# Optimization experiments

Hardware: AMD Instinct MI355X
Metric: run time of the kernel (lower is better)

## Reference

```python
import jax, jax.numpy as jnp
import numpy as np

D = 768
SCALE = 1.0 / np.sqrt(D)  # 1/sqrt(question_size)
NEG_INF = -1e30


def setup_inputs() -> dict:
    key = jax.random.key(0)
    k1, k2, k3, k4 = jax.random.split(key, 4)
    B, Lc, Lq = 8, 2048, 1024
    context_hiddens = jax.random.normal(k1, (B, Lc, D), dtype=jnp.float32)
    context_mask = jnp.ones((B, Lc), dtype=jnp.float32)  # unused by forward (parity with original)
    question_hiddens = jax.random.normal(k2, (B, Lq, D), dtype=jnp.float32)
    question_mask = jax.random.randint(k3, (B, Lq), 0, 2, dtype=jnp.int32)
    # ensure at least one valid question token per row to avoid all -inf softmax
    question_mask = question_mask.at[:, 0].set(1)
    W = jax.random.normal(k4, (D, D), dtype=jnp.float32) * (1.0 / np.sqrt(D))
    b = jnp.zeros((D,), dtype=jnp.float32)
    return {
        "context_hiddens": context_hiddens,
        "context_mask": context_mask,
        "question_hiddens": question_hiddens,
        "question_mask": question_mask,
        "W": W,
        "b": b,
    }


def reference(context_hiddens, context_mask, question_hiddens, question_mask, W, b):
    # Linear projection of question hiddens: [B, Lq, D]
    query = jnp.einsum("bqd,ed->bqe", question_hiddens, W) + b
    # Bilinear scores: c_i' W q_j -> [B, Lc, Lq], scaled
    scores = jnp.einsum("bcd,bqd->bcq", context_hiddens, query) * SCALE
    # Masked softmax over question axis (mask==1 means valid)
    mask = question_mask[:, None, :].astype(jnp.bool_)  # [B, 1, Lq]
    scores = jnp.where(mask, scores, NEG_INF)
    attention_dist = jax.nn.softmax(scores, axis=2)
    # Weighted sum of question hiddens: [B, Lc, D]
    attn_output = jnp.einsum("bcq,bqd->bcd", attention_dist, question_hiddens)
    return jnp.concatenate([context_hiddens, attn_output], axis=2)  # [B, Lc, 2D]
```

## Files before the change

### kernel.cpp

```cpp
#include <hip/hip_runtime.h>
#include <hip/hip_bf16.h>
#include <cstdint>
#include <cstddef>

#define D 768
#define BATCH 8
#define LC 2048
#define LQ 1024
#define SCALE 0.03608439182435161f

typedef __attribute__((ext_vector_type(8))) short short8;
typedef __attribute__((ext_vector_type(4))) float floatx4;

__device__ __forceinline__ short f2bf(float f) {
    union { float f; uint32_t u; } v; v.f = f;
    uint32_t r = v.u + 0x7fffu + ((v.u >> 16) & 1u);
    return (short)(r >> 16);
}

__device__ __forceinline__ void gl_lds16(const short* g, short* l) {
    __builtin_amdgcn_global_load_lds(
        reinterpret_cast<const __attribute__((address_space(1))) unsigned int*>(
            reinterpret_cast<uintptr_t>(g)),
        reinterpret_cast<__attribute__((address_space(3))) unsigned int*>(
            reinterpret_cast<uintptr_t>(l)),
        16, 0, 0);
}

__device__ __forceinline__ void stage_tile(const short* gbase, int ld, int m0, int k0,
                                           short* lds, int tid) {
    const int r = tid >> 2, kc = (tid & 3) * 8;
    gl_lds16(gbase + (size_t)(m0 + r) * ld + k0 + kc, lds + tid * 8);
    gl_lds16(gbase + (size_t)(m0 + r + 64) * ld + k0 + kc, lds + 2048 + tid * 8);
}

__device__ __forceinline__ void mfma_tile_loop(
    const short* Ab, const short* Bb, int lda, int ldb, int K, int m0, int n0,
    short* sA, short* sB, int tid, floatx4 acc[4][4]) {
    const int w = tid >> 6, lane = tid & 63, l15 = lane & 15, quad = lane >> 4;
    const int wm = (w >> 1) * 64, wn = (w & 1) * 64;
    for (int k0 = 0; k0 < K; k0 += 32) {
        stage_tile(Ab, lda, m0, k0, sA, tid);
        stage_tile(Bb, ldb, n0, k0, sB, tid);
        __syncthreads();
        short8 af[4], bf[4];
#pragma unroll
        for (int mt = 0; mt < 4; ++mt)
            af[mt] = *reinterpret_cast<const short8*>(&sA[(wm + mt * 16 + l15) * 32 + quad * 8]);
#pragma unroll
        for (int nt = 0; nt < 4; ++nt)
            bf[nt] = *reinterpret_cast<const short8*>(&sB[(wn + nt * 16 + l15) * 32 + quad * 8]);
#pragma unroll
        for (int mt = 0; mt < 4; ++mt)
#pragma unroll
            for (int nt = 0; nt < 4; ++nt)
                acc[mt][nt] = __builtin_amdgcn_mfma_f32_16x16x32_bf16(af[mt], bf[nt], acc[mt][nt], 0, 0, 0);
        __syncthreads();
    }
}

__device__ __forceinline__ void gemm256_loop(
    const short* __restrict__ A, const short* __restrict__ B,
    int lda, int ldb, int K, int m0, int n0,
    short* lds, int tid, floatx4 acc[8][4]) {
    const int lane = tid & 63, l15 = lane & 15, quad = lane >> 4;
    const int w = tid >> 6, wm = w >> 2, wn = w & 3;

    const int c0 = tid, c1 = tid + 512;
    const int r0 = c0 >> 2, s0 = (c0 & 3) ^ (r0 & 3);
    const int r1 = c1 >> 2, s1 = (c1 & 3) ^ (r1 & 3);
    const short* gA0 = A + (size_t)(m0 + r0) * lda + s0 * 8;
    const short* gA1 = A + (size_t)(m0 + r1) * lda + s1 * 8;
    const short* gB0 = B + (size_t)(n0 + r0) * ldb + s0 * 8;
    const short* gB1 = B + (size_t)(n0 + r1) * ldb + s1 * 8;
    short* dA0 = lds + c0 * 8;
    short* dA1 = lds + c1 * 8;
    short* dB0 = lds + 8192 + c0 * 8;
    short* dB1 = lds + 8192 + c1 * 8;

    int aoff[8], boff[4];
#pragma unroll
    for (int mt = 0; mt < 8; ++mt) {
        int r = wm * 128 + mt * 16 + l15;
        aoff[mt] = r * 32 + ((quad ^ (r & 3)) * 8);
    }
#pragma unroll
    for (int nt = 0; nt < 4; ++nt) {
        int r = wn * 64 + nt * 16 + l15;
        boff[nt] = 8192 + r * 32 + ((quad ^ (r & 3)) * 8);
    }

    const int NT = K >> 5;
#define STAGE_A(t, bb) { gl_lds16(gA0 + (t) * 32, dA0 + (bb)); gl_lds16(gA1 + (t) * 32, dA1 + (bb)); }
#define STAGE_B(t, bb) { gl_lds16(gB0 + (t) * 32, dB0 + (bb)); gl_lds16(gB1 + (t) * 32, dB1 + (bb)); }
    STAGE_A(0, 0) STAGE_B(0, 0)
    STAGE_A(1, 16384) STAGE_B(1, 16384)

    for (int kt = 0; kt < NT; ++kt) {
        const int cur = (kt % 3) * 16384;
        const int nxt = ((kt + 2) % 3) * 16384;
        if (kt + 1 < NT) { asm volatile("s_waitcnt vmcnt(4)" ::: "memory"); }
        else             { asm volatile("s_waitcnt vmcnt(0)" ::: "memory"); }
        __builtin_amdgcn_s_barrier();
        __builtin_amdgcn_sched_barrier(0);

        if (kt + 2 < NT) STAGE_A((kt + 2), nxt)

        short8 af[8], bf[4];
#pragma unroll
        for (int mt = 0; mt < 8; ++mt)
            af[mt] = *reinterpret_cast<const short8*>(lds + cur + aoff[mt]);
#pragma unroll
        for (int nt = 0; nt < 2; ++nt)
            bf[nt] = *reinterpret_cast<const short8*>(lds + cur + boff[nt]);
        __builtin_amdgcn_s_setprio(1);
#pragma unroll
        for (int mt = 0; mt < 8; ++mt)
#pragma unroll
            for (int nt = 0; nt < 2; ++nt)
                acc[mt][nt] = __builtin_amdgcn_mfma_f32_16x16x32_bf16(af[mt], bf[nt], acc[mt][nt], 0, 0, 0);
        __builtin_amdgcn_s_setprio(0);

        if (kt + 2 < NT) STAGE_B((kt + 2), nxt)

#pragma unroll
        for (int nt = 2; nt < 4; ++nt)
            bf[nt] = *reinterpret_cast<const short8*>(lds + cur + boff[nt]);
        __builtin_amdgcn_s_setprio(1);
#pragma unroll
        for (int mt = 0; mt < 8; ++mt)
#pragma unroll
            for (int nt = 2; nt < 4; ++nt)
                acc[mt][nt] = __builtin_amdgcn_mfma_f32_16x16x32_bf16(af[mt], bf[nt], acc[mt][nt], 0, 0, 0);
        __builtin_amdgcn_s_setprio(0);
        __builtin_amdgcn_sched_barrier(0);
    }
#undef STAGE_A
#undef STAGE_B
}

__global__ void cast_w_kernel(const float* __restrict__ src, short* __restrict__ dst,
                              float* __restrict__ sums) {
    int i = blockIdx.x * 256 + threadIdx.x;
    if (i < 4096) {
        float4 z = {0.f, 0.f, 0.f, 0.f};
        reinterpret_cast<float4*>(sums)[i] = z;
    }
    float4 v = reinterpret_cast<const float4*>(src)[i];
    short4 o;
    o.x = f2bf(v.x); o.y = f2bf(v.y); o.z = f2bf(v.z); o.w = f2bf(v.w);
    reinterpret_cast<short4*>(dst)[i] = o;
}

__global__ void qh_pass_kernel(const float* __restrict__ qh, short* __restrict__ qh_b,
                               short* __restrict__ qhT) {
    __shared__ float tile[32][33];
    const int b = blockIdx.z;
    const int q0 = blockIdx.x * 32, d0 = blockIdx.y * 32;
    const int t = threadIdx.x;
    const int r = t >> 3, c = (t & 7) * 4;
    const float4 v = *reinterpret_cast<const float4*>(qh + ((size_t)b * LQ + q0 + r) * D + d0 + c);
    tile[r][c] = v.x; tile[r][c + 1] = v.y; tile[r][c + 2] = v.z; tile[r][c + 3] = v.w;
    short4 d;
    d.x = f2bf(v.x); d.y = f2bf(v.y); d.z = f2bf(v.z); d.w = f2bf(v.w);
    *reinterpret_cast<short4*>(qh_b + ((size_t)b * LQ + q0 + r) * D + d0 + c) = d;
    __syncthreads();
    short4 o;
    o.x = f2bf(tile[c][r]); o.y = f2bf(tile[c + 1][r]);
    o.z = f2bf(tile[c + 2][r]); o.w = f2bf(tile[c + 3][r]);
    *reinterpret_cast<short4*>(qhT + ((size_t)b * D + d0 + r) * LQ + q0 + c) = o;
}

__global__ __launch_bounds__(256, 2) void gemm1_kernel(
    const short* __restrict__ A, const short* __restrict__ W,
    const float* __restrict__ bias, short* __restrict__ Q) {
    __shared__ short sA[128 * 32];
    __shared__ short sB[128 * 32];
    const int m0 = blockIdx.x * 128, n0 = blockIdx.y * 128;
    const int tid = threadIdx.x;
    const int w = tid >> 6, lane = tid & 63, l15 = lane & 15, quad = lane >> 4;
    const int wm = (w >> 1) * 64, wn = (w & 1) * 64;
    floatx4 acc[4][4];
#pragma unroll
    for (int i = 0; i < 4; ++i)
#pragma unroll
        for (int j = 0; j < 4; ++j) { floatx4 z = {0.f, 0.f, 0.f, 0.f}; acc[i][j] = z; }
    mfma_tile_loop(A, W, D, D, D, m0, n0, sA, sB, tid, acc);
    float bv[4];
#pragma unroll
    for (int nt = 0; nt < 4; ++nt) bv[nt] = bias[n0 + wn + nt * 16 + l15];
#pragma unroll
    for (int mt = 0; mt < 4; ++mt)
#pragma unroll
        for (int r = 0; r < 4; ++r) {
            int row = m0 + wm + mt * 16 + quad * 4 + r;
#pragma unroll
            for (int nt = 0; nt < 4; ++nt)
                Q[(size_t)row * D + n0 + wn + nt * 16 + l15] = f2bf(acc[mt][nt][r] + bv[nt]);
        }
}

__global__ void ctx_pass_kernel(const float* __restrict__ ctx, float* __restrict__ out,
                                short* __restrict__ ctxb) {
    size_t i = (size_t)blockIdx.x * 256 + threadIdx.x;
    size_t row = i / 192;
    size_t c4 = i % 192;
    float4 v = reinterpret_cast<const float4*>(ctx)[i];
    reinterpret_cast<float4*>(out)[row * 384 + c4] = v;
    short4 o;
    o.x = f2bf(v.x); o.y = f2bf(v.y); o.z = f2bf(v.z); o.w = f2bf(v.w);
    reinterpret_cast<short4*>(ctxb)[i] = o;
}

__global__ __launch_bounds__(512, 2) void scores256_kernel(
    const short* __restrict__ ctxb, const short* __restrict__ query_b,
    const int* __restrict__ qmask, short* __restrict__ P, float* __restrict__ sums) {
    __shared__ __align__(16) short lds[3 * 16384];
    const int nb = ((blockIdx.x & 7) << 5) + (blockIdx.x >> 3);
    const int b = nb >> 5, rem = nb & 31, by = rem >> 3, bx = rem & 7;
    const int m0 = bx << 8, n0 = by << 8;
    const int tid = threadIdx.x;
    const int lane = tid & 63, l15 = lane & 15, quad = lane >> 4;
    const int w = tid >> 6, wm = w >> 2, wn = w & 3;

    floatx4 acc[8][4];
#pragma unroll
    for (int i = 0; i < 8; ++i)
#pragma unroll
        for (int j = 0; j < 4; ++j) { floatx4 z = {0.f, 0.f, 0.f, 0.f}; acc[i][j] = z; }

    gemm256_loop(ctxb + (size_t)b * LC * D, query_b + (size_t)b * LQ * D,
                 D, D, D, m0, n0, lds, tid, acc);

    const int* mk = qmask + b * LQ;
    bool valid[4];
#pragma unroll
    for (int nt = 0; nt < 4; ++nt) valid[nt] = (mk[n0 + wn * 64 + nt * 16 + l15] != 0);
    short* Pb = P + (size_t)b * LC * LQ;
    float* sumb = sums + (size_t)b * LC;
#pragma unroll
    for (int mt = 0; mt < 8; ++mt)
#pragma unroll
        for (int rr = 0; rr < 4; ++rr) {
            int row = m0 + wm * 128 + mt * 16 + quad * 4 + rr;
            float psum = 0.f;
#pragma unroll
            for (int nt = 0; nt < 4; ++nt) {
                float pv = valid[nt] ? __expf(acc[mt][nt][rr] * SCALE) : 0.f;
                psum += pv;
                Pb[(size_t)row * LQ + n0 + wn * 64 + nt * 16 + l15] = f2bf(pv);
            }
#pragma unroll
            for (int off = 1; off < 16; off <<= 1)
                psum += __shfl_xor(psum, off, 64);
            if (l15 == 0)
                atomicAdd(&sumb[row], psum);
        }
}

__global__ __launch_bounds__(512, 2) void gemm2_256_kernel(
    const short* __restrict__ P, const short* __restrict__ qhT,
    const float* __restrict__ sums, float* __restrict__ out) {
    __shared__ __align__(16) short lds[3 * 16384];
    const int nb = (blockIdx.x & 7) * 24 + (blockIdx.x >> 3);
    const int b = nb / 24, rem = nb % 24, by = rem >> 3, bx = rem & 7;
    const int m0 = bx << 8, n0 = by << 8;
    const int tid = threadIdx.x;
    const int lane = tid & 63, l15 = lane & 15, quad = lane >> 4;
    const int w = tid >> 6, wm = w >> 2, wn = w & 3;

    floatx4 acc[8][4];
#pragma unroll
    for (int i = 0; i < 8; ++i)
#pragma unroll
        for (int j = 0; j < 4; ++j) { floatx4 z = {0.f, 0.f, 0.f, 0.f}; acc[i][j] = z; }

    gemm256_loop(P + (size_t)b * LC * LQ, qhT + (size_t)b * D * LQ,
                 LQ, LQ, LQ, m0, n0, lds, tid, acc);

    const float* sumb = sums + (size_t)b * LC;
#pragma unroll
    for (int mt = 0; mt < 8; ++mt)
#pragma unroll
        for (int rr = 0; rr < 4; ++rr) {
            int lrow = m0 + wm * 128 + mt * 16 + quad * 4 + rr;
            const float inv = 1.0f / sumb[lrow];
            size_t rowoff = ((size_t)b * LC + lrow) * 1536 + 768;
#pragma unroll
            for (int nt = 0; nt < 4; ++nt)
                out[rowoff + n0 + wn * 64 + nt * 16 + l15] = acc[mt][nt][rr] * inv;
        }
}

extern "C" void kernel_launch(void* const* d_in, const int* in_sizes, int n_in,
                              void* d_out, int out_size, void* d_ws, size_t ws_size,
                              hipStream_t stream) {
    const float* ctx = (const float*)d_in[0];
    const float* qh = (const float*)d_in[2];
    const int* qmask = (const int*)d_in[3];
    const float* Wf = (const float*)d_in[4];
    const float* bias = (const float*)d_in[5];
    float* out = (float*)d_out;

    char* ws = (char*)d_ws;
    short* W_b     = (short*)(ws);
    short* query_b = (short*)(ws + 1179648);
    short* qhT     = (short*)(ws + 13762560);
    short* ctx_b   = (short*)(ws + 26345472);
    short* P       = (short*)(ws + 51511296);
    float* sums    = (float*)(ws + 85065728);
    short* qh_b    = (short*)(ws + 51511296);

    cast_w_kernel<<<576, 256, 0, stream>>>(Wf, W_b, sums);
    qh_pass_kernel<<<dim3(32, 24, 8), 256, 0, stream>>>(qh, qh_b, qhT);
    ctx_pass_kernel<<<12288, 256, 0, stream>>>(ctx, out, ctx_b);
    gemm1_kernel<<<dim3(64, 6), 256, 0, stream>>>(qh_b, W_b, bias, query_b);
    scores256_kernel<<<dim3(256), dim3(512), 0, stream>>>(ctx_b, query_b, qmask, P, sums);
    gemm2_256_kernel<<<dim3(192), dim3(512), 0, stream>>>(P, qhT, sums, out);
}
```

Baseline: 265.8 us.

## Fuse prep kernels and switch GEMMs to 128x256 tiles with higher occupancy

Merges the three cast/transpose/copy kernels into a single prep kernel, which removes launch overhead. All three GEMMs move to a shared 128x256 triple-buffered pipeline. Scores and gemm2 shrink from 256x256 tiles, so they launch twice as many blocks across the CUs, and gemm1 moves from the simple synchronous loop onto the pipelined one. The costs are lower per-block arithmetic reuse, more redundant loads of the B operand, and reliance on 4 blocks per CU fitting in registers and LDS.

```diff
diff --git a/kernel.cpp b/kernel.cpp
--- a/kernel.cpp
+++ b/kernel.cpp
@@ -27,95 +27,62 @@
         16, 0, 0);
 }
 
-__device__ __forceinline__ void stage_tile(const short* gbase, int ld, int m0, int k0,
-                                           short* lds, int tid) {
-    const int r = tid >> 2, kc = (tid & 3) * 8;
-    gl_lds16(gbase + (size_t)(m0 + r) * ld + k0 + kc, lds + tid * 8);
-    gl_lds16(gbase + (size_t)(m0 + r + 64) * ld + k0 + kc, lds + 2048 + tid * 8);
-}
-
-__device__ __forceinline__ void mfma_tile_loop(
-    const short* Ab, const short* Bb, int lda, int ldb, int K, int m0, int n0,
-    short* sA, short* sB, int tid, floatx4 acc[4][4]) {
-    const int w = tid >> 6, lane = tid & 63, l15 = lane & 15, quad = lane >> 4;
-    const int wm = (w >> 1) * 64, wn = (w & 1) * 64;
-    for (int k0 = 0; k0 < K; k0 += 32) {
-        stage_tile(Ab, lda, m0, k0, sA, tid);
-        stage_tile(Bb, ldb, n0, k0, sB, tid);
-        __syncthreads();
-        short8 af[4], bf[4];
-#pragma unroll
-        for (int mt = 0; mt < 4; ++mt)
-            af[mt] = *reinterpret_cast<const short8*>(&sA[(wm + mt * 16 + l15) * 32 + quad * 8]);
-#pragma unroll
-        for (int nt = 0; nt < 4; ++nt)
-            bf[nt] = *reinterpret_cast<const short8*>(&sB[(wn + nt * 16 + l15) * 32 + quad * 8]);
-#pragma unroll
-        for (int mt = 0; mt < 4; ++mt)
-#pragma unroll
-            for (int nt = 0; nt < 4; ++nt)
-                acc[mt][nt] = __builtin_amdgcn_mfma_f32_16x16x32_bf16(af[mt], bf[nt], acc[mt][nt], 0, 0, 0);
-        __syncthreads();
-    }
-}
-
-__device__ __forceinline__ void gemm256_loop(
+__device__ __forceinline__ void gemm128x256_loop(
     const short* __restrict__ A, const short* __restrict__ B,
     int lda, int ldb, int K, int m0, int n0,
-    short* lds, int tid, floatx4 acc[8][4]) {
-    const int lane = tid & 63, l15 = lane & 15, quad = lane >> 4;
-    const int w = tid >> 6, wm = w >> 2, wn = w & 3;
-
-    const int c0 = tid, c1 = tid + 512;
-    const int r0 = c0 >> 2, s0 = (c0 & 3) ^ (r0 & 3);
-    const int r1 = c1 >> 2, s1 = (c1 & 3) ^ (r1 & 3);
-    const short* gA0 = A + (size_t)(m0 + r0) * lda + s0 * 8;
-    const short* gA1 = A + (size_t)(m0 + r1) * lda + s1 * 8;
-    const short* gB0 = B + (size_t)(n0 + r0) * ldb + s0 * 8;
-    const short* gB1 = B + (size_t)(n0 + r1) * ldb + s1 * 8;
-    short* dA0 = lds + c0 * 8;
-    short* dA1 = lds + c1 * 8;
-    short* dB0 = lds + 8192 + c0 * 8;
-    short* dB1 = lds + 8192 + c1 * 8;
-
-    int aoff[8], boff[4];
-#pragma unroll
-    for (int mt = 0; mt < 8; ++mt) {
-        int r = wm * 128 + mt * 16 + l15;
+    short* lds, int tid, floatx4 acc[4][4]) {
+    const int lane = tid & 63, l15 = lane & 15, quad = lane >> 4;
+    const int w = tid >> 6, wm = w >> 2, wn = w & 3;
+
+    const int ra = tid >> 2, sa = (tid & 3) ^ (ra & 3);
+    const short* gA = A + (size_t)(m0 + ra) * lda + sa * 8;
+    short* dA = lds + tid * 8;
+    const int cb0 = tid, cb1 = tid + 512;
+    const int rb0 = cb0 >> 2, sb0 = (cb0 & 3) ^ (rb0 & 3);
+    const int rb1 = cb1 >> 2, sb1 = (cb1 & 3) ^ (rb1 & 3);
+    const short* gB0 = B + (size_t)(n0 + rb0) * ldb + sb0 * 8;
+    const short* gB1 = B + (size_t)(n0 + rb1) * ldb + sb1 * 8;
+    short* dB0 = lds + 4096 + cb0 * 8;
+    short* dB1 = lds + 4096 + cb1 * 8;
+
+    int aoff[4], boff[4];
+#pragma unroll
+    for (int mt = 0; mt < 4; ++mt) {
+        int r = wm * 64 + mt * 16 + l15;
         aoff[mt] = r * 32 + ((quad ^ (r & 3)) * 8);
     }
 #pragma unroll
     for (int nt = 0; nt < 4; ++nt) {
         int r = wn * 64 + nt * 16 + l15;
-        boff[nt] = 8192 + r * 32 + ((quad ^ (r & 3)) * 8);
+        boff[nt] = 4096 + r * 32 + ((quad ^ (r & 3)) * 8);
     }
 
     const int NT = K >> 5;
-#define STAGE_A(t, bb) { gl_lds16(gA0 + (t) * 32, dA0 + (bb)); gl_lds16(gA1 + (t) * 32, dA1 + (bb)); }
+#define STAGE_A(t, bb) { gl_lds16(gA + (t) * 32, dA + (bb)); }
 #define STAGE_B(t, bb) { gl_lds16(gB0 + (t) * 32, dB0 + (bb)); gl_lds16(gB1 + (t) * 32, dB1 + (bb)); }
     STAGE_A(0, 0) STAGE_B(0, 0)
-    STAGE_A(1, 16384) STAGE_B(1, 16384)
+    STAGE_A(1, 12288) STAGE_B(1, 12288)
 
     for (int kt = 0; kt < NT; ++kt) {
-        const int cur = (kt % 3) * 16384;
-        const int nxt = ((kt + 2) % 3) * 16384;
-        if (kt + 1 < NT) { asm volatile("s_waitcnt vmcnt(4)" ::: "memory"); }
+        const int cur = (kt % 3) * 12288;
+        const int nxt = ((kt + 2) % 3) * 12288;
+        if (kt + 1 < NT) { asm volatile("s_waitcnt vmcnt(3)" ::: "memory"); }
         else             { asm volatile("s_waitcnt vmcnt(0)" ::: "memory"); }
         __builtin_amdgcn_s_barrier();
         __builtin_amdgcn_sched_barrier(0);
 
         if (kt + 2 < NT) STAGE_A((kt + 2), nxt)
 
-        short8 af[8], bf[4];
-#pragma unroll
-        for (int mt = 0; mt < 8; ++mt)
+        short8 af[4], bf[4];
+#pragma unroll
+        for (int mt = 0; mt < 4; ++mt)
             af[mt] = *reinterpret_cast<const short8*>(lds + cur + aoff[mt]);
 #pragma unroll
         for (int nt = 0; nt < 2; ++nt)
             bf[nt] = *reinterpret_cast<const short8*>(lds + cur + boff[nt]);
         __builtin_amdgcn_s_setprio(1);
 #pragma unroll
-        for (int mt = 0; mt < 8; ++mt)
+        for (int mt = 0; mt < 4; ++mt)
 #pragma unroll
             for (int nt = 0; nt < 2; ++nt)
                 acc[mt][nt] = __builtin_amdgcn_mfma_f32_16x16x32_bf16(af[mt], bf[nt], acc[mt][nt], 0, 0, 0);
@@ -128,7 +95,7 @@
             bf[nt] = *reinterpret_cast<const short8*>(lds + cur + boff[nt]);
         __builtin_amdgcn_s_setprio(1);
 #pragma unroll
-        for (int mt = 0; mt < 8; ++mt)
+        for (int mt = 0; mt < 4; ++mt)
 #pragma unroll
             for (int nt = 2; nt < 4; ++nt)
                 acc[mt][nt] = __builtin_amdgcn_mfma_f32_16x16x32_bf16(af[mt], bf[nt], acc[mt][nt], 0, 0, 0);
@@ -139,99 +106,103 @@
 #undef STAGE_B
 }
 
-__global__ void cast_w_kernel(const float* __restrict__ src, short* __restrict__ dst,
-                              float* __restrict__ sums) {
-    int i = blockIdx.x * 256 + threadIdx.x;
-    if (i < 4096) {
+__global__ __launch_bounds__(256) void prep_kernel(
+    const float* __restrict__ ctx, const float* __restrict__ qh,
+    const float* __restrict__ Wf, float* __restrict__ out,
+    short* __restrict__ W_b, short* __restrict__ ctx_b,
+    short* __restrict__ qh_b, short* __restrict__ qhT, float* __restrict__ sums) {
+    __shared__ float tile[32][33];
+    const int tid = threadIdx.x;
+    const int bid = blockIdx.x;
+    const int gid = bid * 256 + tid;
+
+    if (gid < 147456) {
+        float4 v = reinterpret_cast<const float4*>(Wf)[gid];
+        short4 o;
+        o.x = f2bf(v.x); o.y = f2bf(v.y); o.z = f2bf(v.z); o.w = f2bf(v.w);
+        reinterpret_cast<short4*>(W_b)[gid] = o;
+    }
+    if (gid < 4096) {
         float4 z = {0.f, 0.f, 0.f, 0.f};
-        reinterpret_cast<float4*>(sums)[i] = z;
-    }
-    float4 v = reinterpret_cast<const float4*>(src)[i];
-    short4 o;
-    o.x = f2bf(v.x); o.y = f2bf(v.y); o.z = f2bf(v.z); o.w = f2bf(v.w);
-    reinterpret_cast<short4*>(dst)[i] = o;
-}
-
-__global__ void qh_pass_kernel(const float* __restrict__ qh, short* __restrict__ qh_b,
-                               short* __restrict__ qhT) {
-    __shared__ float tile[32][33];
-    const int b = blockIdx.z;
-    const int q0 = blockIdx.x * 32, d0 = blockIdx.y * 32;
-    const int t = threadIdx.x;
-    const int r = t >> 3, c = (t & 7) * 4;
-    const float4 v = *reinterpret_cast<const float4*>(qh + ((size_t)b * LQ + q0 + r) * D + d0 + c);
-    tile[r][c] = v.x; tile[r][c + 1] = v.y; tile[r][c + 2] = v.z; tile[r][c + 3] = v.w;
-    short4 d;
-    d.x = f2bf(v.x); d.y = f2bf(v.y); d.z = f2bf(v.z); d.w = f2bf(v.w);
-    *reinterpret_cast<short4*>(qh_b + ((size_t)b * LQ + q0 + r) * D + d0 + c) = d;
-    __syncthreads();
-    short4 o;
-    o.x = f2bf(tile[c][r]); o.y = f2bf(tile[c + 1][r]);
-    o.z = f2bf(tile[c + 2][r]); o.w = f2bf(tile[c + 3][r]);
-    *reinterpret_cast<short4*>(qhT + ((size_t)b * D + d0 + r) * LQ + q0 + c) = o;
-}
-
-__global__ __launch_bounds__(256, 2) void gemm1_kernel(
+        reinterpret_cast<float4*>(sums)[gid] = z;
+    }
+#pragma unroll
+    for (int it = 0; it < 6; ++it) {
+        int i = gid + it * 524288;
+        int row = i / 192, c4 = i % 192;
+        float4 v = reinterpret_cast<const float4*>(ctx)[i];
+        reinterpret_cast<float4*>(out)[(size_t)row * 384 + c4] = v;
+        short4 o;
+        o.x = f2bf(v.x); o.y = f2bf(v.y); o.z = f2bf(v.z); o.w = f2bf(v.w);
+        reinterpret_cast<short4*>(ctx_b)[i] = o;
+    }
+    const int r = tid >> 3, c = (tid & 7) * 4;
+#pragma unroll
+    for (int it = 0; it < 3; ++it) {
+        const int T = bid + it * 2048;
+        const int b = T / 768, rem = T % 768;
+        const int q0 = (rem / 24) * 32, d0 = (rem % 24) * 32;
+        const float4 v = *reinterpret_cast<const float4*>(
+            qh + ((size_t)b * LQ + q0 + r) * D + d0 + c);
+        tile[r][c] = v.x; tile[r][c + 1] = v.y; tile[r][c + 2] = v.z; tile[r][c + 3] = v.w;
+        short4 d;
+        d.x = f2bf(v.x); d.y = f2bf(v.y); d.z = f2bf(v.z); d.w = f2bf(v.w);
+        *reinterpret_cast<short4*>(qh_b + ((size_t)b * LQ + q0 + r) * D + d0 + c) = d;
+        __syncthreads();
+        short4 o;
+        o.x = f2bf(tile[c][r]); o.y = f2bf(tile[c + 1][r]);
+        o.z = f2bf(tile[c + 2][r]); o.w = f2bf(tile[c + 3][r]);
+        *reinterpret_cast<short4*>(qhT + ((size_t)b * D + d0 + r) * LQ + q0 + c) = o;
+        __syncthreads();
+    }
+}
+
+__global__ __launch_bounds__(512, 4) void gemm1_kernel(
     const short* __restrict__ A, const short* __restrict__ W,
     const float* __restrict__ bias, short* __restrict__ Q) {
-    __shared__ short sA[128 * 32];
-    __shared__ short sB[128 * 32];
-    const int m0 = blockIdx.x * 128, n0 = blockIdx.y * 128;
-    const int tid = threadIdx.x;
-    const int w = tid >> 6, lane = tid & 63, l15 = lane & 15, quad = lane >> 4;
-    const int wm = (w >> 1) * 64, wn = (w & 1) * 64;
+    __shared__ __align__(16) short lds[3 * 12288];
+    const int nb = (blockIdx.x & 7) * 24 + (blockIdx.x >> 3);
+    const int m0 = (nb / 3) * 128, n0 = (nb % 3) * 256;
+    const int tid = threadIdx.x;
+    const int lane = tid & 63, l15 = lane & 15, quad = lane >> 4;
+    const int w = tid >> 6, wm = w >> 2, wn = w & 3;
     floatx4 acc[4][4];
 #pragma unroll
     for (int i = 0; i < 4; ++i)
 #pragma unroll
         for (int j = 0; j < 4; ++j) { floatx4 z = {0.f, 0.f, 0.f, 0.f}; acc[i][j] = z; }
-    mfma_tile_loop(A, W, D, D, D, m0, n0, sA, sB, tid, acc);
+    gemm128x256_loop(A, W, D, D, D, m0, n0, lds, tid, acc);
     float bv[4];
 #pragma unroll
-    for (int nt = 0; nt < 4; ++nt) bv[nt] = bias[n0 + wn + nt * 16 + l15];
+    for (int nt = 0; nt < 4; ++nt) bv[nt] = bias[n0 + wn * 64 + nt * 16 + l15];
 #pragma unroll
     for (int mt = 0; mt < 4; ++mt)
 #pragma unroll
-        for (int r = 0; r < 4; ++r) {
-            int row = m0 + wm + mt * 16 + quad * 4 + r;
+        for (int rr = 0; rr < 4; ++rr) {
+            int row = m0 + wm * 64 + mt * 16 + quad * 4 + rr;
 #pragma unroll
             for (int nt = 0; nt < 4; ++nt)
-                Q[(size_t)row * D + n0 + wn + nt * 16 + l15] = f2bf(acc[mt][nt][r] + bv[nt]);
+                Q[(size_t)row * D + n0 + wn * 64 + nt * 16 + l15] = f2bf(acc[mt][nt][rr] + bv[nt]);
         }
 }
 
-__global__ void ctx_pass_kernel(const float* __restrict__ ctx, float* __restrict__ out,
-                                short* __restrict__ ctxb) {
-    size_t i = (size_t)blockIdx.x * 256 + threadIdx.x;
-    size_t row = i / 192;
-    size_t c4 = i % 192;
-    float4 v = reinterpret_cast<const float4*>(ctx)[i];
-    reinterpret_cast<float4*>(out)[row * 384 + c4] = v;
-    short4 o;
-    o.x = f2bf(v.x); o.y = f2bf(v.y); o.z = f2bf(v.z); o.w = f2bf(v.w);
-    reinterpret_cast<short4*>(ctxb)[i] = o;
-}
-
-__global__ __launch_bounds__(512, 2) void scores256_kernel(
+__global__ __launch_bounds__(512, 4) void scores_kernel(
     const short* __restrict__ ctxb, const short* __restrict__ query_b,
     const int* __restrict__ qmask, short* __restrict__ P, float* __restrict__ sums) {
-    __shared__ __align__(16) short lds[3 * 16384];
-    const int nb = ((blockIdx.x & 7) << 5) + (blockIdx.x >> 3);
-    const int b = nb >> 5, rem = nb & 31, by = rem >> 3, bx = rem & 7;
-    const int m0 = bx << 8, n0 = by << 8;
-    const int tid = threadIdx.x;
-    const int lane = tid & 63, l15 = lane & 15, quad = lane >> 4;
-    const int w = tid >> 6, wm = w >> 2, wn = w & 3;
-
-    floatx4 acc[8][4];
-#pragma unroll
-    for (int i = 0; i < 8; ++i)
+    __shared__ __align__(16) short lds[3 * 12288];
+    const int nb = ((blockIdx.x & 7) << 6) + (blockIdx.x >> 3);
+    const int b = nb >> 6, rem = nb & 63, bx = rem >> 2, by = rem & 3;
+    const int m0 = bx << 7, n0 = by << 8;
+    const int tid = threadIdx.x;
+    const int lane = tid & 63, l15 = lane & 15, quad = lane >> 4;
+    const int w = tid >> 6, wm = w >> 2, wn = w & 3;
+    floatx4 acc[4][4];
+#pragma unroll
+    for (int i = 0; i < 4; ++i)
 #pragma unroll
         for (int j = 0; j < 4; ++j) { floatx4 z = {0.f, 0.f, 0.f, 0.f}; acc[i][j] = z; }
-
-    gemm256_loop(ctxb + (size_t)b * LC * D, query_b + (size_t)b * LQ * D,
-                 D, D, D, m0, n0, lds, tid, acc);
-
+    gemm128x256_loop(ctxb + (size_t)b * LC * D, query_b + (size_t)b * LQ * D,
+                     D, D, D, m0, n0, lds, tid, acc);
     const int* mk = qmask + b * LQ;
     bool valid[4];
 #pragma unroll
@@ -239,10 +210,10 @@
     short* Pb = P + (size_t)b * LC * LQ;
     float* sumb = sums + (size_t)b * LC;
 #pragma unroll
-    for (int mt = 0; mt < 8; ++mt)
+    for (int mt = 0; mt < 4; ++mt)
 #pragma unroll
         for (int rr = 0; rr < 4; ++rr) {
-            int row = m0 + wm * 128 + mt * 16 + quad * 4 + rr;
+            int row = m0 + wm * 64 + mt * 16 + quad * 4 + rr;
             float psum = 0.f;
 #pragma unroll
             for (int nt = 0; nt < 4; ++nt) {
@@ -258,32 +229,29 @@
         }
 }
 
-__global__ __launch_bounds__(512, 2) void gemm2_256_kernel(
+__global__ __launch_bounds__(512, 4) void gemm2_kernel(
     const short* __restrict__ P, const short* __restrict__ qhT,
     const float* __restrict__ sums, float* __restrict__ out) {
-    __shared__ __align__(16) short lds[3 * 16384];
-    const int nb = (blockIdx.x & 7) * 24 + (blockIdx.x >> 3);
-    const int b = nb / 24, rem = nb % 24, by = rem >> 3, bx = rem & 7;
-    const int m0 = bx << 8, n0 = by << 8;
-    const int tid = threadIdx.x;
-    const int lane = tid & 63, l15 = lane & 15, quad = lane >> 4;
-    const int w = tid >> 6, wm = w >> 2, wn = w & 3;
-
-    floatx4 acc[8][4];
-#pragma unroll
-    for (int i = 0; i < 8; ++i)
+    __shared__ __align__(16) short lds[3 * 12288];
+    const int nb = (blockIdx.x & 7) * 48 + (blockIdx.x >> 3);
+    const int b = nb / 48, rem = nb % 48, bx = rem / 3, by = rem % 3;
+    const int m0 = bx << 7, n0 = by << 8;
+    const int tid = threadIdx.x;
+    const int lane = tid & 63, l15 = lane & 15, quad = lane >> 4;
+    const int w = tid >> 6, wm = w >> 2, wn = w & 3;
+    floatx4 acc[4][4];
+#pragma unroll
+    for (int i = 0; i < 4; ++i)
 #pragma unroll
         for (int j = 0; j < 4; ++j) { floatx4 z = {0.f, 0.f, 0.f, 0.f}; acc[i][j] = z; }
-
-    gemm256_loop(P + (size_t)b * LC * LQ, qhT + (size_t)b * D * LQ,
-                 LQ, LQ, LQ, m0, n0, lds, tid, acc);
-
+    gemm128x256_loop(P + (size_t)b * LC * LQ, qhT + (size_t)b * D * LQ,
+                     LQ, LQ, LQ, m0, n0, lds, tid, acc);
     const float* sumb = sums + (size_t)b * LC;
 #pragma unroll
-    for (int mt = 0; mt < 8; ++mt)
+    for (int mt = 0; mt < 4; ++mt)
 #pragma unroll
         for (int rr = 0; rr < 4; ++rr) {
-            int lrow = m0 + wm * 128 + mt * 16 + quad * 4 + rr;
+            int lrow = m0 + wm * 64 + mt * 16 + quad * 4 + rr;
             const float inv = 1.0f / sumb[lrow];
             size_t rowoff = ((size_t)b * LC + lrow) * 1536 + 768;
 #pragma unroll
@@ -311,10 +279,8 @@
     float* sums    = (float*)(ws + 85065728);
     short* qh_b    = (short*)(ws + 51511296);
 
-    cast_w_kernel<<<576, 256, 0, stream>>>(Wf, W_b, sums);
-    qh_pass_kernel<<<dim3(32, 24, 8), 256, 0, stream>>>(qh, qh_b, qhT);
-    ctx_pass_kernel<<<12288, 256, 0, stream>>>(ctx, out, ctx_b);
-    gemm1_kernel<<<dim3(64, 6), 256, 0, stream>>>(qh_b, W_b, bias, query_b);
-    scores256_kernel<<<dim3(256), dim3(512), 0, stream>>>(ctx_b, query_b, qmask, P, sums);
-    gemm2_256_kernel<<<dim3(192), dim3(512), 0, stream>>>(P, qhT, sums, out);
-}
+    prep_kernel<<<2048, 256, 0, stream>>>(ctx, qh, Wf, out, W_b, ctx_b, qh_b, qhT, sums);
+    gemm1_kernel<<<192, 512, 0, stream>>>(qh_b, W_b, bias, query_b);
+    scores_kernel<<<512, 512, 0, stream>>>(ctx_b, query_b, qmask, P, sums);
+    gemm2_kernel<<<384, 512, 0, stream>>>(P, qhT, sums, out);
+}
```

Result: no change. 269.2 us (+1.3%).
